# Optimization experiments

Measured on AMD Instinct MI355X. Metric: run time of the kernel, lower is better.

Reference implementation:

```python
import jax, jax.numpy as jnp
import numpy as np

IN_DIMS = 1024
K = 8


def setup_inputs() -> dict:
    key = jax.random.key(0)
    ks = jax.random.split(key, 7)
    s = 1.0 / np.sqrt(IN_DIMS)
    x = jax.random.normal(ks[0], (8, 2048, IN_DIMS), dtype=jnp.float32)
    Wq = jax.random.uniform(ks[1], (IN_DIMS, K), jnp.float32, -s, s)
    bq = jax.random.uniform(ks[2], (K,), jnp.float32, -s, s)
    Wk = jax.random.uniform(ks[3], (IN_DIMS, K), jnp.float32, -s, s)
    bk = jax.random.uniform(ks[4], (K,), jnp.float32, -s, s)
    Wv = jax.random.uniform(ks[5], (IN_DIMS, IN_DIMS), jnp.float32, -s, s)
    bv = jax.random.uniform(ks[6], (IN_DIMS,), jnp.float32, -s, s)
    return {"x": x, "Wq": Wq, "bq": bq, "Wk": Wk, "bk": bk, "Wv": Wv, "bv": bv}


def reference(x, Wq, bq, Wk, bk, Wv, bv):
    # x: [B,S,D]; rank-k projections
    q = jnp.einsum('bsd,dk->bsk', x, Wq) + bq        # [B,S,k]
    k = jnp.einsum('bsd,dk->bsk', x, Wk) + bk        # [B,S,k]
    energy = jnp.einsum('bik,bjk->bij', q, k)        # [B,S,S] (unscaled)
    attention = jax.nn.softmax(energy, axis=-1)
    value = jnp.einsum('bsd,de->bse', x, Wv) + bv    # [B,S,D]
    out = jnp.einsum('bij,bjd->bid', attention, value)
    return (out, attention)
```

## Files before the change

kernel.cpp:

```cpp
#include <hip/hip_runtime.h>


typedef __attribute__((ext_vector_type(8))) __bf16 bf16x8;
typedef __attribute__((ext_vector_type(4))) __bf16 bf16x4;
typedef __attribute__((ext_vector_type(4))) float  f32x4;
typedef unsigned int u32;

#define GLB_CAST(p) ((const __attribute__((address_space(1))) u32*)(p))
#define LDS_CAST(p) ((__attribute__((address_space(3))) u32*)(p))

#define S_BARRIER() { __builtin_amdgcn_s_barrier(); __builtin_amdgcn_sched_barrier(0); }
#define VMCNT8()    { asm volatile("s_waitcnt vmcnt(8)" ::: "memory"); __builtin_amdgcn_sched_barrier(0); }
#define VMCNT0()    { asm volatile("s_waitcnt vmcnt(0)" ::: "memory"); __builtin_amdgcn_sched_barrier(0); }

static constexpr int    Bn   = 8;
static constexpr int    S    = 2048;
static constexpr int    Dd   = 1024;
static constexpr int    Mtot = Bn * S;
static constexpr size_t OUT0 = (size_t)Bn * S * Dd;

static constexpr size_t OFF_XBF  = 0;
static constexpr size_t OFF_WVT  = OFF_XBF + (size_t)Mtot * Dd * 2;
static constexpr size_t OFF_Q    = OFF_WVT + (size_t)Dd * Dd * 2;
static constexpr size_t OFF_K    = OFF_Q   + (size_t)Mtot * 8 * 4;
static constexpr size_t OFF_VT   = OFF_K   + (size_t)Mtot * 8 * 4;
static constexpr size_t OFF_ATTB = OFF_VT  + (size_t)Bn * Dd * S * 2;
static constexpr size_t WS_NEED  = OFF_ATTB + (size_t)Bn * S * S * 2;

__global__ __launch_bounds__(256) void prep_kernel(
    const float* __restrict__ x, const float* __restrict__ Wq,
    const float* __restrict__ Wk, const float* __restrict__ Wv,
    const float* __restrict__ bq, const float* __restrict__ bk,
    __bf16* __restrict__ xbf, __bf16* __restrict__ wvt,
    float* __restrict__ qb, float* __restrict__ kb)
{
    __shared__ float lt[64][65];
    int bid = blockIdx.x, t = threadIdx.x;
    if (bid < 256) {
        int l = t & 63, w = t >> 6;
        int mbase = (bid * 4 + w) * 16;
        int n = l & 15;
        int dbase = (l >> 4) << 3;
        const float* xr = x + (size_t)(mbase + n) * 1024 + dbase;
        const float* wcol = (n < 8) ? (Wq + n) : (Wk + (n & 7));
        f32x4 acc = {0.f, 0.f, 0.f, 0.f};
        #pragma unroll 4
        for (int kk = 0; kk < 1024; kk += 32) {
            f32x4 a0 = *(const f32x4*)(xr + kk);
            f32x4 a1 = *(const f32x4*)(xr + kk + 4);
            bf16x8 a, b;
            #pragma unroll
            for (int c = 0; c < 4; ++c) { a[c] = (__bf16)a0[c]; a[4 + c] = (__bf16)a1[c]; }
            #pragma unroll
            for (int u = 0; u < 8; ++u) b[u] = (__bf16)wcol[(size_t)(dbase + kk + u) * 8];
            acc = __builtin_amdgcn_mfma_f32_16x16x32_bf16(a, b, acc, 0, 0, 0);
        }
        float bias = (n < 8) ? bq[n] : bk[n & 7];
        #pragma unroll
        for (int r = 0; r < 4; ++r) {
            int m = mbase + ((l >> 4) << 2) + r;
            float v = acc[r] + bias;
            if (n < 8) qb[m * 8 + n] = v;
            else       kb[m * 8 + (n & 7)] = v;
        }
    } else if (bid < 512) {
        int tile = bid - 256;
        int tr = tile >> 4, tc = tile & 15;
        int r0 = t >> 6, c = t & 63;
        #pragma unroll
        for (int i = 0; i < 16; ++i) {
            int row = i * 4 + r0;
            lt[row][c] = Wv[(size_t)(tr * 64 + row) * 1024 + tc * 64 + c];
        }
        __syncthreads();
        #pragma unroll
        for (int i = 0; i < 16; ++i) {
            int er = i * 4 + r0;
            wvt[(size_t)(tc * 64 + er) * 1024 + tr * 64 + c] = (__bf16)lt[c][er];
        }
    } else {
        int bid2 = bid - 512;
        #pragma unroll
        for (int i = 0; i < 4; ++i) {
            size_t idx4 = (size_t)i * 1048576 + (size_t)bid2 * 256 + t;
            f32x4 v = ((const f32x4*)x)[idx4];
            bf16x4 o;
            #pragma unroll
            for (int c = 0; c < 4; ++c) o[c] = (__bf16)v[c];
            ((bf16x4*)xbf)[idx4] = o;
        }
    }
}

__global__ __launch_bounds__(256) void softmax_kernel(
    const float* __restrict__ qb, const float* __restrict__ kb,
    float* __restrict__ attnF, __bf16* __restrict__ attnB)
{
    int bid = blockIdx.x;
    int b = bid >> 6, chunk = bid & 63;
    int t = threadIdx.x, l = t & 63, w = t >> 6;
    float kr[8][8];
    const float* kbb = kb + ((size_t)b << 14);
    #pragma unroll
    for (int jj = 0; jj < 8; ++jj) {
        f32x4 v0 = *(const f32x4*)(kbb + (size_t)(t * 8 + jj) * 8);
        f32x4 v1 = *(const f32x4*)(kbb + (size_t)(t * 8 + jj) * 8 + 4);
        #pragma unroll
        for (int c = 0; c < 4; ++c) { kr[jj][c] = v0[c]; kr[jj][4 + c] = v1[c]; }
    }
    __shared__ float redm[4], reds[4];
    const float* qrow = qb + ((size_t)b << 14);
    for (int ii = 0; ii < 32; ++ii) {
        int i = (chunk << 5) + ii;
        f32x4 q0 = *(const f32x4*)(qrow + (size_t)i * 8);
        f32x4 q1 = *(const f32x4*)(qrow + (size_t)i * 8 + 4);
        float e[8];
        #pragma unroll
        for (int jj = 0; jj < 8; ++jj) {
            float s = q0[0] * kr[jj][0];
            s = fmaf(q0[1], kr[jj][1], s);
            s = fmaf(q0[2], kr[jj][2], s);
            s = fmaf(q0[3], kr[jj][3], s);
            s = fmaf(q1[0], kr[jj][4], s);
            s = fmaf(q1[1], kr[jj][5], s);
            s = fmaf(q1[2], kr[jj][6], s);
            s = fmaf(q1[3], kr[jj][7], s);
            e[jj] = s;
        }
        float mx = e[0];
        #pragma unroll
        for (int jj = 1; jj < 8; ++jj) mx = fmaxf(mx, e[jj]);
        #pragma unroll
        for (int d = 1; d < 64; d <<= 1) mx = fmaxf(mx, __shfl_xor(mx, d));
        if (l == 0) redm[w] = mx;
        __syncthreads();
        mx = fmaxf(fmaxf(redm[0], redm[1]), fmaxf(redm[2], redm[3]));
        float p[8], sum = 0.f;
        #pragma unroll
        for (int jj = 0; jj < 8; ++jj) { p[jj] = __expf(e[jj] - mx); sum += p[jj]; }
        #pragma unroll
        for (int d = 1; d < 64; d <<= 1) sum += __shfl_xor(sum, d);
        if (l == 0) reds[w] = sum;
        __syncthreads();
        float T = (reds[0] + reds[1]) + (reds[2] + reds[3]);
        float inv = 1.0f / T;
        size_t off = (((size_t)b << 11) + i) * 2048 + (size_t)t * 8;
        f32x4 o0, o1; bf16x8 ob;
        #pragma unroll
        for (int c = 0; c < 4; ++c) {
            o0[c] = p[c] * inv; o1[c] = p[4 + c] * inv;
            ob[c] = (__bf16)o0[c]; ob[4 + c] = (__bf16)o1[c];
        }
        *(f32x4*)(attnF + off) = o0;
        *(f32x4*)(attnF + off + 4) = o1;
        *(bf16x8*)(attnB + off) = ob;
    }
}

template<int MODE>
__global__ __launch_bounds__(512, 2) void gemm_kernel(
    const __bf16* __restrict__ A, const __bf16* __restrict__ Bt,
    float* __restrict__ outF, __bf16* __restrict__ outVt,
    const float* __restrict__ bv)
{
    constexpr int LDA = (MODE == 0) ? 1024 : 2048;
    constexpr int NT  = LDA / 64;
    __shared__ __align__(1024) char smem[131072];

    int bid = blockIdx.x;
    int wg = ((bid & 7) << 5) | (bid >> 3);
    int t = threadIdx.x, l = t & 63;
    int wid = t >> 6;
    int wmr = wid >> 2, wnc = wid & 3;

    int mblk, nblk, bb = 0;
    size_t aoff, boff;
    if constexpr (MODE == 0) {
        mblk = wg >> 2; nblk = wg & 3;
        aoff = (size_t)mblk * 256 * LDA; boff = 0;
    } else {
        bb = wg >> 5; int r = wg & 31;
        mblk = r >> 2; nblk = r & 3;
        aoff = (size_t)bb * S * S + (size_t)mblk * 256 * LDA;
        boff = (size_t)bb * Dd * S;
    }
    const __bf16* Ab = A + aoff;
    const __bf16* Bb = Bt + boff + (size_t)nblk * 256 * LDA;

    int rowin = t >> 3;
    int sl8 = (t & 7) ^ (rowin & 7);
    int lr = l & 15, lk = l >> 4;

    int slot0 = (lk ^ (lr & 7)) << 3;
    int slot1 = ((lk ^ 4) ^ (lr & 7)) << 3;
    int offA0 = (wmr * 128 + lr) * 64 + slot0;
    int offA1 = (wmr * 128 + lr) * 64 + slot1;
    int offB0 = (wnc * 64 + lr) * 64 + slot0;
    int offB1 = (wnc * 64 + lr) * 64 + slot1;

    const __bf16* gA[4]; const __bf16* gB[4];
    #pragma unroll
    for (int c = 0; c < 4; ++c) {
        gA[c] = Ab + (size_t)(c * 64 + rowin) * LDA + sl8 * 8;
        gB[c] = Bb + (size_t)(c * 64 + rowin) * LDA + sl8 * 8;
    }

    f32x4 acc[8][4] = {};

    #pragma unroll
    for (int c = 0; c < 4; ++c) {
        __builtin_amdgcn_global_load_lds(GLB_CAST(gA[c]),
            LDS_CAST(smem + c * 8192 + wid * 1024), 16, 0, 0);
        __builtin_amdgcn_global_load_lds(GLB_CAST(gB[c]),
            LDS_CAST(smem + 32768 + c * 8192 + wid * 1024), 16, 0, 0);
    }
    #pragma unroll
    for (int c = 0; c < 4; ++c) {
        __builtin_amdgcn_global_load_lds(GLB_CAST(gA[c] + 64),
            LDS_CAST(smem + 65536 + c * 8192 + wid * 1024), 16, 0, 0);
        __builtin_amdgcn_global_load_lds(GLB_CAST(gB[c] + 64),
            LDS_CAST(smem + 65536 + 32768 + c * 8192 + wid * 1024), 16, 0, 0);
    }
    VMCNT8();
    S_BARRIER();

    for (int tt = 0; tt < NT; ++tt) {
        const __bf16* Asl = (const __bf16*)(smem + ((tt & 1) << 16));
        const __bf16* Bsl = Asl + 16384;
        bf16x8 af[8], bfr[4];

        #pragma unroll
        for (int i = 0; i < 8; ++i) af[i] = *(const bf16x8*)(Asl + offA0 + i * 1024);
        #pragma unroll
        for (int j = 0; j < 4; ++j) bfr[j] = *(const bf16x8*)(Bsl + offB0 + j * 1024);
        __builtin_amdgcn_s_setprio(1);
        #pragma unroll
        for (int i = 0; i < 8; ++i)
            #pragma unroll
            for (int j = 0; j < 4; ++j)
                acc[i][j] = __builtin_amdgcn_mfma_f32_16x16x32_bf16(af[i], bfr[j], acc[i][j], 0, 0, 0);
        __builtin_amdgcn_s_setprio(0);

        #pragma unroll
        for (int i = 0; i < 8; ++i) af[i] = *(const bf16x8*)(Asl + offA1 + i * 1024);
        #pragma unroll
        for (int j = 0; j < 4; ++j) bfr[j] = *(const bf16x8*)(Bsl + offB1 + j * 1024);
        __builtin_amdgcn_s_setprio(1);
        #pragma unroll
        for (int i = 0; i < 8; ++i)
            #pragma unroll
            for (int j = 0; j < 4; ++j)
                acc[i][j] = __builtin_amdgcn_mfma_f32_16x16x32_bf16(af[i], bfr[j], acc[i][j], 0, 0, 0);
        __builtin_amdgcn_s_setprio(0);

        if (tt == NT - 1) break;
        S_BARRIER();
        if (tt + 2 < NT) {
            int kk2 = (tt + 2) * 64;
            char* dst = smem + ((tt & 1) << 16);
            #pragma unroll
            for (int c = 0; c < 4; ++c) {
                __builtin_amdgcn_global_load_lds(GLB_CAST(gA[c] + kk2),
                    LDS_CAST(dst + c * 8192 + wid * 1024), 16, 0, 0);
                __builtin_amdgcn_global_load_lds(GLB_CAST(gB[c] + kk2),
                    LDS_CAST(dst + 32768 + c * 8192 + wid * 1024), 16, 0, 0);
            }
            VMCNT8();
        } else {
            VMCNT0();
        }
        S_BARRIER();
    }

    int lr2 = l & 15, lk2 = l >> 4;
    if constexpr (MODE == 0) {
        #pragma unroll
        for (int j = 0; j < 4; ++j) {
            int e = (nblk << 8) + wnc * 64 + j * 16 + lr2;
            float bias = bv[e];
            #pragma unroll
            for (int i = 0; i < 8; ++i) {
                int m0 = (mblk << 8) + wmr * 128 + i * 16 + (lk2 << 2);
                int b = m0 >> 11, s0 = m0 & 2047;
                bf16x4 o;
                #pragma unroll
                for (int r = 0; r < 4; ++r) o[r] = (__bf16)(acc[i][j][r] + bias);
                *(bf16x4*)&outVt[(((size_t)(b << 10) + e) << 11) + s0] = o;
            }
        }
    } else {
        float* ob = outF + (size_t)bb * S * Dd;
        #pragma unroll
        for (int i = 0; i < 8; ++i) {
            int m0 = (mblk << 8) + wmr * 128 + i * 16 + (lk2 << 2);
            #pragma unroll
            for (int j = 0; j < 4; ++j) {
                int e = (nblk << 8) + wnc * 64 + j * 16 + lr2;
                #pragma unroll
                for (int r = 0; r < 4; ++r)
                    ob[(size_t)(m0 + r) * 1024 + e] = acc[i][j][r];
            }
        }
    }
}

extern "C" void kernel_launch(void* const* d_in, const int* in_sizes, int n_in,
                              void* d_out, int out_size, void* d_ws, size_t ws_size,
                              hipStream_t stream)
{
    const float* x  = (const float*)d_in[0];
    const float* Wq = (const float*)d_in[1];
    const float* bq = (const float*)d_in[2];
    const float* Wk = (const float*)d_in[3];
    const float* bk = (const float*)d_in[4];
    const float* Wv = (const float*)d_in[5];
    const float* bv = (const float*)d_in[6];

    float* outp  = (float*)d_out;
    float* attnF = outp + OUT0;

    if (ws_size < WS_NEED) return;
    char* ws = (char*)d_ws;
    __bf16* xbf   = (__bf16*)(ws + OFF_XBF);
    __bf16* wvt   = (__bf16*)(ws + OFF_WVT);
    float*  qbuf  = (float*)(ws + OFF_Q);
    float*  kbuf  = (float*)(ws + OFF_K);
    __bf16* vt    = (__bf16*)(ws + OFF_VT);
    __bf16* attnB = (__bf16*)(ws + OFF_ATTB);

    prep_kernel<<<4608, 256, 0, stream>>>(x, Wq, Wk, Wv, bq, bk, xbf, wvt, qbuf, kbuf);
    gemm_kernel<0><<<256, 512, 0, stream>>>(xbf, wvt, nullptr, vt, bv);
    softmax_kernel<<<512, 256, 0, stream>>>(qbuf, kbuf, attnF, attnB);
    gemm_kernel<1><<<256, 512, 0, stream>>>(attnB, vt, outp, nullptr, nullptr);
}
```

Baseline: 200.1 us.

## Shrink GEMM tiles to 256x128 with BK=32, and stage the Vt epilogue through LDS

The GEMM kernels move from 512-thread 256x256 tiles with BK=64 to 256-thread 256x128 tiles with BK=32. This doubles the grid to 512 blocks and cuts LDS per block, so more blocks fit per CU. The swizzle is reworked for the narrower K slice. The transposed-V epilogue now writes through swizzled LDS, so global stores are contiguous 16-byte chunks instead of scattered bf16x4 writes. In exchange, each K step has fewer MFMAs per barrier and each CU reuses less data.

Result: slower. 209.0 us (+4.4%).

```diff
diff --git a/kernel.cpp b/kernel.cpp
--- a/kernel.cpp
+++ b/kernel.cpp
@@ -10,7 +10,7 @@
 #define LDS_CAST(p) ((__attribute__((address_space(3))) u32*)(p))
 
 #define S_BARRIER() { __builtin_amdgcn_s_barrier(); __builtin_amdgcn_sched_barrier(0); }
-#define VMCNT8()    { asm volatile("s_waitcnt vmcnt(8)" ::: "memory"); __builtin_amdgcn_sched_barrier(0); }
+#define VMCNT6()    { asm volatile("s_waitcnt vmcnt(6)" ::: "memory"); __builtin_amdgcn_sched_barrier(0); }
 #define VMCNT0()    { asm volatile("s_waitcnt vmcnt(0)" ::: "memory"); __builtin_amdgcn_sched_barrier(0); }
 
 static constexpr int    Bn   = 8;
@@ -158,81 +158,77 @@
 }
 
 template<int MODE>
-__global__ __launch_bounds__(512, 2) void gemm_kernel(
+__global__ __launch_bounds__(256, 2) void gemm_kernel(
     const __bf16* __restrict__ A, const __bf16* __restrict__ Bt,
     float* __restrict__ outF, __bf16* __restrict__ outVt,
     const float* __restrict__ bv)
 {
     constexpr int LDA = (MODE == 0) ? 1024 : 2048;
-    constexpr int NT  = LDA / 64;
-    __shared__ __align__(1024) char smem[131072];
+    constexpr int NT  = LDA / 32;
+    __shared__ __align__(1024) char smem[(MODE == 0) ? 65536 : 49152];
 
     int bid = blockIdx.x;
-    int wg = ((bid & 7) << 5) | (bid >> 3);
+    int wg = ((bid & 7) << 6) | (bid >> 3);
     int t = threadIdx.x, l = t & 63;
     int wid = t >> 6;
-    int wmr = wid >> 2, wnc = wid & 3;
+    int wmr = wid >> 1, wnc = wid & 1;
 
     int mblk, nblk, bb = 0;
     size_t aoff, boff;
     if constexpr (MODE == 0) {
-        mblk = wg >> 2; nblk = wg & 3;
-        aoff = (size_t)mblk * 256 * LDA; boff = 0;
+        mblk = wg >> 3; nblk = wg & 7;
+        aoff = (size_t)mblk * 256 * LDA;
+        boff = (size_t)nblk * 128 * LDA;
     } else {
-        bb = wg >> 5; int r = wg & 31;
-        mblk = r >> 2; nblk = r & 3;
+        bb = wg >> 6; int rr = wg & 63;
+        mblk = rr >> 3; nblk = rr & 7;
         aoff = (size_t)bb * S * S + (size_t)mblk * 256 * LDA;
-        boff = (size_t)bb * Dd * S;
-    }
-    const __bf16* Ab = A + aoff;
-    const __bf16* Bb = Bt + boff + (size_t)nblk * 256 * LDA;
-
-    int rowin = t >> 3;
-    int sl8 = (t & 7) ^ (rowin & 7);
+        boff = (size_t)bb * Dd * S + (size_t)nblk * 128 * LDA;
+    }
+
+    int presw = (t & 3) ^ ((t >> 3) & 3);
+    const __bf16* gA[4]; const __bf16* gB[2];
+    #pragma unroll
+    for (int c = 0; c < 4; ++c)
+        gA[c] = A + aoff + (size_t)(c * 64 + (t >> 2)) * LDA + presw * 8;
+    #pragma unroll
+    for (int c = 0; c < 2; ++c)
+        gB[c] = Bt + boff + (size_t)(c * 64 + (t >> 2)) * LDA + presw * 8;
+
     int lr = l & 15, lk = l >> 4;
-
-    int slot0 = (lk ^ (lr & 7)) << 3;
-    int slot1 = ((lk ^ 4) ^ (lr & 7)) << 3;
-    int offA0 = (wmr * 128 + lr) * 64 + slot0;
-    int offA1 = (wmr * 128 + lr) * 64 + slot1;
-    int offB0 = (wnc * 64 + lr) * 64 + slot0;
-    int offB1 = (wnc * 64 + lr) * 64 + slot1;
-
-    const __bf16* gA[4]; const __bf16* gB[4];
-    #pragma unroll
-    for (int c = 0; c < 4; ++c) {
-        gA[c] = Ab + (size_t)(c * 64 + rowin) * LDA + sl8 * 8;
-        gB[c] = Bb + (size_t)(c * 64 + rowin) * LDA + sl8 * 8;
-    }
+    int fsl = (lk ^ ((lr >> 1) & 3)) << 3;
+    int offA = (wmr * 128 + lr) * 32 + fsl;
+    int offB = (wnc * 64 + lr) * 32 + fsl;
 
     f32x4 acc[8][4] = {};
 
     #pragma unroll
-    for (int c = 0; c < 4; ++c) {
+    for (int c = 0; c < 4; ++c)
         __builtin_amdgcn_global_load_lds(GLB_CAST(gA[c]),
-            LDS_CAST(smem + c * 8192 + wid * 1024), 16, 0, 0);
+            LDS_CAST(smem + c * 4096 + t * 16), 16, 0, 0);
+    #pragma unroll
+    for (int c = 0; c < 2; ++c)
         __builtin_amdgcn_global_load_lds(GLB_CAST(gB[c]),
-            LDS_CAST(smem + 32768 + c * 8192 + wid * 1024), 16, 0, 0);
-    }
-    #pragma unroll
-    for (int c = 0; c < 4; ++c) {
-        __builtin_amdgcn_global_load_lds(GLB_CAST(gA[c] + 64),
-            LDS_CAST(smem + 65536 + c * 8192 + wid * 1024), 16, 0, 0);
-        __builtin_amdgcn_global_load_lds(GLB_CAST(gB[c] + 64),
-            LDS_CAST(smem + 65536 + 32768 + c * 8192 + wid * 1024), 16, 0, 0);
-    }
-    VMCNT8();
+            LDS_CAST(smem + 16384 + c * 4096 + t * 16), 16, 0, 0);
+    #pragma unroll
+    for (int c = 0; c < 4; ++c)
+        __builtin_amdgcn_global_load_lds(GLB_CAST(gA[c] + 32),
+            LDS_CAST(smem + 24576 + c * 4096 + t * 16), 16, 0, 0);
+    #pragma unroll
+    for (int c = 0; c < 2; ++c)
+        __builtin_amdgcn_global_load_lds(GLB_CAST(gB[c] + 32),
+            LDS_CAST(smem + 24576 + 16384 + c * 4096 + t * 16), 16, 0, 0);
+    VMCNT6();
     S_BARRIER();
 
     for (int tt = 0; tt < NT; ++tt) {
-        const __bf16* Asl = (const __bf16*)(smem + ((tt & 1) << 16));
-        const __bf16* Bsl = Asl + 16384;
+        const __bf16* Asl = (const __bf16*)(smem + (tt & 1) * 24576);
+        const __bf16* Bsl = Asl + 8192;
         bf16x8 af[8], bfr[4];
-
-        #pragma unroll
-        for (int i = 0; i < 8; ++i) af[i] = *(const bf16x8*)(Asl + offA0 + i * 1024);
-        #pragma unroll
-        for (int j = 0; j < 4; ++j) bfr[j] = *(const bf16x8*)(Bsl + offB0 + j * 1024);
+        #pragma unroll
+        for (int i = 0; i < 8; ++i) af[i] = *(const bf16x8*)(Asl + offA + i * 512);
+        #pragma unroll
+        for (int j = 0; j < 4; ++j) bfr[j] = *(const bf16x8*)(Bsl + offB + j * 512);
         __builtin_amdgcn_s_setprio(1);
         #pragma unroll
         for (int i = 0; i < 8; ++i)
@@ -241,61 +237,63 @@
                 acc[i][j] = __builtin_amdgcn_mfma_f32_16x16x32_bf16(af[i], bfr[j], acc[i][j], 0, 0, 0);
         __builtin_amdgcn_s_setprio(0);
 
-        #pragma unroll
-        for (int i = 0; i < 8; ++i) af[i] = *(const bf16x8*)(Asl + offA1 + i * 1024);
-        #pragma unroll
-        for (int j = 0; j < 4; ++j) bfr[j] = *(const bf16x8*)(Bsl + offB1 + j * 1024);
-        __builtin_amdgcn_s_setprio(1);
-        #pragma unroll
-        for (int i = 0; i < 8; ++i)
-            #pragma unroll
-            for (int j = 0; j < 4; ++j)
-                acc[i][j] = __builtin_amdgcn_mfma_f32_16x16x32_bf16(af[i], bfr[j], acc[i][j], 0, 0, 0);
-        __builtin_amdgcn_s_setprio(0);
-
         if (tt == NT - 1) break;
         S_BARRIER();
         if (tt + 2 < NT) {
-            int kk2 = (tt + 2) * 64;
-            char* dst = smem + ((tt & 1) << 16);
-            #pragma unroll
-            for (int c = 0; c < 4; ++c) {
+            int kk2 = (tt + 2) * 32;
+            char* dst = smem + (tt & 1) * 24576;
+            #pragma unroll
+            for (int c = 0; c < 4; ++c)
                 __builtin_amdgcn_global_load_lds(GLB_CAST(gA[c] + kk2),
-                    LDS_CAST(dst + c * 8192 + wid * 1024), 16, 0, 0);
+                    LDS_CAST(dst + c * 4096 + t * 16), 16, 0, 0);
+            #pragma unroll
+            for (int c = 0; c < 2; ++c)
                 __builtin_amdgcn_global_load_lds(GLB_CAST(gB[c] + kk2),
-                    LDS_CAST(dst + 32768 + c * 8192 + wid * 1024), 16, 0, 0);
-            }
-            VMCNT8();
+                    LDS_CAST(dst + 16384 + c * 4096 + t * 16), 16, 0, 0);
+            VMCNT6();
         } else {
             VMCNT0();
         }
         S_BARRIER();
     }
 
-    int lr2 = l & 15, lk2 = l >> 4;
     if constexpr (MODE == 0) {
+        S_BARRIER();
         #pragma unroll
         for (int j = 0; j < 4; ++j) {
-            int e = (nblk << 8) + wnc * 64 + j * 16 + lr2;
-            float bias = bv[e];
+            int e_loc = wnc * 64 + j * 16 + lr;
+            float bias = bv[(nblk << 7) + e_loc];
             #pragma unroll
             for (int i = 0; i < 8; ++i) {
-                int m0 = (mblk << 8) + wmr * 128 + i * 16 + (lk2 << 2);
-                int b = m0 >> 11, s0 = m0 & 2047;
+                int slot = wmr * 16 + i * 2 + (lk >> 1);
                 bf16x4 o;
                 #pragma unroll
                 for (int r = 0; r < 4; ++r) o[r] = (__bf16)(acc[i][j][r] + bias);
-                *(bf16x4*)&outVt[(((size_t)(b << 10) + e) << 11) + s0] = o;
+                *(bf16x4*)(smem + e_loc * 512 + ((slot ^ (e_loc & 7)) << 4) + (lk & 1) * 8) = o;
+            }
+        }
+        S_BARRIER();
+        int b = mblk >> 3, sbase = (mblk & 7) << 8;
+        #pragma unroll
+        for (int u = 0; u < 8; ++u) {
+            int e_loc = u * 16 + (t >> 4);
+            int e_glob = (nblk << 7) + e_loc;
+            __bf16* dst = outVt + (((size_t)(b << 10) + e_glob) << 11) + sbase;
+            #pragma unroll
+            for (int v = 0; v < 2; ++v) {
+                int sv = (t & 15) + (v << 4);
+                bf16x8 val = *(const bf16x8*)(smem + e_loc * 512 + ((sv ^ (e_loc & 7)) << 4));
+                *(bf16x8*)(dst + sv * 8) = val;
             }
         }
     } else {
         float* ob = outF + (size_t)bb * S * Dd;
         #pragma unroll
         for (int i = 0; i < 8; ++i) {
-            int m0 = (mblk << 8) + wmr * 128 + i * 16 + (lk2 << 2);
+            int m0 = (mblk << 8) + wmr * 128 + i * 16 + (lk << 2);
             #pragma unroll
             for (int j = 0; j < 4; ++j) {
-                int e = (nblk << 8) + wnc * 64 + j * 16 + lr2;
+                int e = (nblk << 7) + wnc * 64 + j * 16 + lr;
                 #pragma unroll
                 for (int r = 0; r < 4; ++r)
                     ob[(size_t)(m0 + r) * 1024 + e] = acc[i][j][r];
@@ -329,7 +327,7 @@
     __bf16* attnB = (__bf16*)(ws + OFF_ATTB);
 
     prep_kernel<<<4608, 256, 0, stream>>>(x, Wq, Wk, Wv, bq, bk, xbf, wvt, qbuf, kbuf);
-    gemm_kernel<0><<<256, 512, 0, stream>>>(xbf, wvt, nullptr, vt, bv);
+    gemm_kernel<0><<<512, 256, 0, stream>>>(xbf, wvt, nullptr, vt, bv);
     softmax_kernel<<<512, 256, 0, stream>>>(qbuf, kbuf, attnF, attnB);
-    gemm_kernel<1><<<256, 512, 0, stream>>>(attnB, vt, outp, nullptr, nullptr);
+    gemm_kernel<1><<<512, 256, 0, stream>>>(attnB, vt, outp, nullptr, nullptr);
 }
```
